# Kernel optimization log

Hardware: AMD Instinct MI355X
Metric: run time of the kernel (lower is better)

The kernel has to match this reference:

```python
import jax, jax.numpy as jnp
import numpy as np

EPS = 1e-5
INV_SQRT2 = 0.7071067811865476

def _rmsnorm(x, w):
    rms = jnp.sqrt(jnp.sum(x * x, axis=-1) / x.shape[-1] + EPS)
    return x / rms[..., None] * w

def _gelu(x):
    # exact erf-based GELU as in the torch module
    return x * (1.0 + jax.scipy.special.erf(x * INV_SQRT2)) * 0.5

def setup_inputs() -> dict:
    key = jax.random.key(0)
    ks = jax.random.split(key, 8)
    B, S, D, DFF = 4, 2048, 1024, 4096
    s = 0.02  # realistic init scale keeps softmax non-degenerate
    return {
        "x": jax.random.normal(ks[0], (B, S, D), jnp.float32),
        "ln1": jax.random.uniform(ks[1], (D,), jnp.float32),
        "ln2": jax.random.uniform(ks[2], (D,), jnp.float32),
        "ffn1": jax.random.normal(ks[3], (DFF, D), jnp.float32) * s,
        "ffn2": jax.random.normal(ks[4], (D, DFF), jnp.float32) * s,
        "k_proj": jax.random.normal(ks[5], (D, D), jnp.float32) * s,
        "q_proj": jax.random.normal(ks[6], (D, D), jnp.float32) * s,
        "v_proj": jax.random.normal(ks[7], (D, D), jnp.float32) * s,
        "out_proj": jax.random.normal(jax.random.fold_in(key, 99), (D, D), jnp.float32) * s,
    }

def reference(x, ln1, ln2, ffn1, ffn2, k_proj, q_proj, v_proj, out_proj):
    S = x.shape[1]
    d_k = x.shape[-1]
    # --- attention branch (single-head, as in source) ---
    h = _rmsnorm(x, ln1)
    Q = h @ q_proj.T  # [B,S,D]
    K = h @ k_proj.T
    V = h @ v_proj.T
    scores = jnp.einsum('bqd,bkd->bqk', Q, K) / jnp.sqrt(jnp.float32(d_k))
    attn = jax.nn.softmax(scores, axis=-1)
    # source: softmax first, then zero out strict-upper (future) entries, renormalize
    causal = jnp.tril(jnp.ones((S, S), jnp.float32))
    attn = attn * causal
    attn = attn / jnp.sum(attn, axis=-1, keepdims=True)
    mh = jnp.einsum('bqk,bkd->bqd', attn, V) @ out_proj
    y = x + mh
    # --- FFN branch: NOTE source feeds RMSNorm2(x), not y ---
    h2 = _rmsnorm(x, ln2)
    ff = _gelu(h2 @ ffn1.T) @ ffn2.T
    return y + ff
```

## Files before the change

### kernel.cpp

```cpp
#include <hip/hip_runtime.h>
#include <math.h>

typedef __bf16 bf16_t;
typedef __bf16 bf16x8 __attribute__((ext_vector_type(8)));
typedef float f32x4 __attribute__((ext_vector_type(4)));

#define LDS16(g, l) __builtin_amdgcn_global_load_lds( \
    (__attribute__((address_space(1))) void*)(g),     \
    (__attribute__((address_space(3))) void*)(l), 16, 0, 0)

__global__ __launch_bounds__(256) void prep_kernel(
    const float* __restrict__ qp, const float* __restrict__ kp,
    const float* __restrict__ vp, const float* __restrict__ f1,
    const float* __restrict__ f2, const float* __restrict__ op,
    const float* __restrict__ x, const float* __restrict__ ln1,
    bf16_t* __restrict__ qkvb, bf16_t* __restrict__ f1b,
    bf16_t* __restrict__ f2b, bf16_t* __restrict__ opT,
    bf16_t* __restrict__ h1)
{
    __shared__ float tile[32][33];
    __shared__ float red[4];
    int bid = blockIdx.x;
    int t = threadIdx.x;
    if (bid < 11264) {
        size_t i = ((size_t)bid * 256 + t) * 4;
        const float* src;
        bf16_t* dst;
        if (i < 3145728) {
            if (i < 1048576)      { src = qp + i;             dst = qkvb + i; }
            else if (i < 2097152) { src = kp + (i - 1048576); dst = qkvb + i; }
            else                  { src = vp + (i - 2097152); dst = qkvb + i; }
        } else if (i < 7340032) { src = f1 + (i - 3145728); dst = f1b + (i - 3145728); }
        else                    { src = f2 + (i - 7340032); dst = f2b + (i - 7340032); }
        float4 v = *(const float4*)src;
        dst[0] = (bf16_t)v.x; dst[1] = (bf16_t)v.y;
        dst[2] = (bf16_t)v.z; dst[3] = (bf16_t)v.w;
    } else if (bid < 12288) {
        int b2 = bid - 11264;
        int c0 = (b2 & 31) * 32, r0 = (b2 >> 5) * 32;
        int tx = t & 31, ty = t >> 5;
#pragma unroll
        for (int i = 0; i < 32; i += 8)
            tile[ty + i][tx] = op[(size_t)(r0 + ty + i) * 1024 + c0 + tx];
        __syncthreads();
#pragma unroll
        for (int i = 0; i < 32; i += 8)
            opT[(size_t)(c0 + ty + i) * 1024 + r0 + tx] = (bf16_t)tile[tx][ty + i];
    } else {
        int row = bid - 12288;
        float4 xv = ((const float4*)(x + (size_t)row * 1024))[t];
        float ss = xv.x * xv.x + xv.y * xv.y + xv.z * xv.z + xv.w * xv.w;
#pragma unroll
        for (int o = 32; o > 0; o >>= 1) ss += __shfl_xor(ss, o, 64);
        if ((t & 63) == 0) red[t >> 6] = ss;
        __syncthreads();
        ss = red[0] + red[1] + red[2] + red[3];
        float rinv = rsqrtf(ss * (1.0f / 1024.0f) + 1e-5f);
        float4 wv = ((const float4*)ln1)[t];
        bf16_t* hp = h1 + (size_t)row * 1024 + t * 4;
        hp[0] = (bf16_t)(xv.x * rinv * wv.x);
        hp[1] = (bf16_t)(xv.y * rinv * wv.y);
        hp[2] = (bf16_t)(xv.z * rinv * wv.z);
        hp[3] = (bf16_t)(xv.w * rinv * wv.w);
    }
}

__global__ __launch_bounds__(256) void rmsnorm_kernel(
    const float* __restrict__ x, const float* __restrict__ w,
    bf16_t* __restrict__ h)
{
    int row = blockIdx.x;
    int t = threadIdx.x;
    float4 xv = ((const float4*)(x + (size_t)row * 1024))[t];
    float ss = xv.x * xv.x + xv.y * xv.y + xv.z * xv.z + xv.w * xv.w;
#pragma unroll
    for (int o = 32; o > 0; o >>= 1) ss += __shfl_xor(ss, o, 64);
    __shared__ float red[4];
    if ((t & 63) == 0) red[t >> 6] = ss;
    __syncthreads();
    ss = red[0] + red[1] + red[2] + red[3];
    float rinv = rsqrtf(ss * (1.0f / 1024.0f) + 1e-5f);
    float4 wv = ((const float4*)w)[t];
    bf16_t* hp = h + (size_t)row * 1024 + t * 4;
    hp[0] = (bf16_t)(xv.x * rinv * wv.x);
    hp[1] = (bf16_t)(xv.y * rinv * wv.y);
    hp[2] = (bf16_t)(xv.z * rinv * wv.z);
    hp[3] = (bf16_t)(xv.w * rinv * wv.w);
}

__global__ __launch_bounds__(256) void transpose_bf16(
    const bf16_t* __restrict__ in, bf16_t* __restrict__ out,
    int rows, int ldin, long long sIn, long long sOut)
{
    __shared__ bf16_t tile[32][33];
    int b = blockIdx.z;
    const bf16_t* ip = in + (long long)b * sIn;
    bf16_t* op = out + (long long)b * sOut;
    int c0 = blockIdx.x * 32, r0 = blockIdx.y * 32;
    int tx = threadIdx.x & 31, ty = threadIdx.x >> 5;
#pragma unroll
    for (int i = 0; i < 32; i += 8)
        tile[ty + i][tx] = ip[(size_t)(r0 + ty + i) * ldin + c0 + tx];
    __syncthreads();
#pragma unroll
    for (int i = 0; i < 32; i += 8)
        op[(size_t)(c0 + ty + i) * rows + r0 + tx] = tile[tx][ty + i];
}

__global__ __launch_bounds__(256) void causal_softmax_kernel(bf16_t* __restrict__ SP)
{
    const int S = 2048;
    int q = blockIdx.x, b = blockIdx.y;
    bf16_t* row = SP + ((size_t)b * S + q) * S;
    int t = threadIdx.x;
    int j0 = t * 8;
    int Jstore = ((q >> 7) + 1) << 7;

    float v[8];
    if (j0 + 7 <= q) {
        bf16x8 xv = *(const bf16x8*)(row + j0);
#pragma unroll
        for (int i = 0; i < 8; i++) v[i] = (float)xv[i];
    } else if (j0 <= q) {
#pragma unroll
        for (int i = 0; i < 8; i++)
            v[i] = (j0 + i <= q) ? (float)row[j0 + i] : -1e30f;
    } else {
#pragma unroll
        for (int i = 0; i < 8; i++) v[i] = -1e30f;
    }

    float mx = v[0];
#pragma unroll
    for (int i = 1; i < 8; i++) mx = fmaxf(mx, v[i]);
#pragma unroll
    for (int o = 32; o > 0; o >>= 1) mx = fmaxf(mx, __shfl_xor(mx, o, 64));
    __shared__ float sm[4], ssum[4];
    if ((t & 63) == 0) sm[t >> 6] = mx;
    __syncthreads();
    mx = fmaxf(fmaxf(sm[0], sm[1]), fmaxf(sm[2], sm[3]));

    float e[8];
    float sum = 0.f;
#pragma unroll
    for (int i = 0; i < 8; i++) {
        e[i] = (v[i] > -1e29f) ? expf(v[i] - mx) : 0.f;
        sum += e[i];
    }
#pragma unroll
    for (int o = 32; o > 0; o >>= 1) sum += __shfl_xor(sum, o, 64);
    if ((t & 63) == 0) ssum[t >> 6] = sum;
    __syncthreads();
    sum = ssum[0] + ssum[1] + ssum[2] + ssum[3];
    float r = 1.0f / sum;

    if (j0 < Jstore) {
        bf16x8 ov;
#pragma unroll
        for (int i = 0; i < 8; i++) ov[i] = (bf16_t)(e[i] * r);
        *(bf16x8*)(row + j0) = ov;
    }
}

template <int EPI, bool CSKIP, bool CKLOOP, bool ASPLIT>
__global__ __launch_bounds__(256) void gemm_bt(
    const bf16_t* __restrict__ A, const bf16_t* __restrict__ A2, int lda,
    const bf16_t* __restrict__ B, int ldb,
    void* Cv, int ldc, const float* R,
    int K, int Ksp, int Mt, long long sA, long long sB, long long sC,
    float scale)
{
    int id = blockIdx.x, bz = blockIdx.z;
    int xcd = id & 7, p = id >> 3;
    int chunk = Mt >> 3;
    int bm = xcd * chunk + (p % chunk);
    int bn = p / chunk;
    if (CSKIP && bn > bm) return;

    __shared__ __align__(16) bf16_t At[128 * 64];
    __shared__ __align__(16) bf16_t Bt[128 * 64];
    int t = threadIdx.x;
    int w = t >> 6, l = t & 63;
    int wm = w >> 1, wn = w & 1;
    int lane_m = l & 15, quad = l >> 4;

    const bf16_t* Ag = A + (long long)bz * sA + (size_t)(bm * 128) * lda;
    const bf16_t* Bg = B + (long long)bz * sB + (size_t)(bn * 128) * ldb;

    int Keff = K;
    if (CKLOOP) {
        int kk = (bm + 1) * 128;
        if (kk < K) Keff = kk;
    }

    f32x4 acc[4][4] = {};

    int rb = w * 8 + (l >> 3);
    int g0 = ((l & 7) ^ ((l >> 3) & 7)) * 8;
    const bf16_t* a0[4];
    const bf16_t* a1[4];
    const bf16_t* b0[4];
#pragma unroll
    for (int j = 0; j < 4; j++) {
        size_t ro = (size_t)(rb + 32 * j);
        a0[j] = Ag + ro * lda + g0;
        if (ASPLIT) a1[j] = A2 + (long long)bz * sA + (size_t)(bm * 128) * lda
                           + ro * lda + g0;
        b0[j] = Bg + ro * ldb + g0;
    }

    int s0 = (quad ^ (lane_m & 7)) * 8;
    int s1 = ((4 + quad) ^ (lane_m & 7)) * 8;

    for (int kt = 0; kt < Keff; kt += 64) {
        __syncthreads();
#pragma unroll
        for (int j = 0; j < 4; j++) {
            const bf16_t* pa = a0[j] + kt;
            if (ASPLIT && kt >= Ksp) pa = a1[j] + (kt - Ksp);
            LDS16(pa, At + (size_t)w * 512 + j * 2048);
            LDS16(b0[j] + kt, Bt + (size_t)w * 512 + j * 2048);
        }
        __syncthreads();

#pragma unroll
        for (int h = 0; h < 2; h++) {
            int sh = h ? s1 : s0;
            bf16x8 af[4], bfr[4];
#pragma unroll
            for (int mi = 0; mi < 4; mi++)
                af[mi] = *(const bf16x8*)(At + (wm * 64 + mi * 16 + lane_m) * 64 + sh);
#pragma unroll
            for (int ni = 0; ni < 4; ni++)
                bfr[ni] = *(const bf16x8*)(Bt + (wn * 64 + ni * 16 + lane_m) * 64 + sh);
#pragma unroll
            for (int mi = 0; mi < 4; mi++)
#pragma unroll
                for (int ni = 0; ni < 4; ni++)
                    acc[mi][ni] = __builtin_amdgcn_mfma_f32_16x16x32_bf16(
                        af[mi], bfr[ni], acc[mi][ni], 0, 0, 0);
        }
    }

    long long cbase = (long long)bz * sC;
#pragma unroll
    for (int mi = 0; mi < 4; mi++) {
#pragma unroll
        for (int r = 0; r < 4; r++) {
            int row = bm * 128 + wm * 64 + mi * 16 + quad * 4 + r;
#pragma unroll
            for (int ni = 0; ni < 4; ni++) {
                int col = bn * 128 + wn * 64 + ni * 16 + lane_m;
                float v = acc[mi][ni][r];
                size_t idx = (size_t)(cbase + (long long)row * ldc + col);
                if (EPI == 0) {
                    ((bf16_t*)Cv)[idx] = (bf16_t)(v * scale);
                } else if (EPI == 1) {
                    float g = 0.5f * v * (1.0f + erff(v * 0.70710678118654752f));
                    ((bf16_t*)Cv)[idx] = (bf16_t)g;
                } else {
                    float rv = R[(size_t)row * ldc + col];
                    ((float*)Cv)[idx] = v + rv;
                }
            }
        }
    }
}

extern "C" void kernel_launch(void* const* d_in, const int* in_sizes, int n_in,
                              void* d_out, int out_size, void* d_ws, size_t ws_size,
                              hipStream_t stream)
{
    (void)in_sizes; (void)n_in; (void)out_size;
    const float* x    = (const float*)d_in[0];
    const float* ln1  = (const float*)d_in[1];
    const float* ln2  = (const float*)d_in[2];
    const float* ffn1 = (const float*)d_in[3];
    const float* ffn2 = (const float*)d_in[4];
    const float* kp   = (const float*)d_in[5];
    const float* qp   = (const float*)d_in[6];
    const float* vp   = (const float*)d_in[7];
    const float* op   = (const float*)d_in[8];
    float* out = (float*)d_out;

    const size_t MiB = 1048576;
    char* ws = (char*)d_ws;
    bf16_t* qkvb = (bf16_t*)(ws + 0 * MiB);
    bf16_t* opT  = (bf16_t*)(ws + 6 * MiB);
    bf16_t* f1b  = (bf16_t*)(ws + 8 * MiB);
    bf16_t* f2b  = (bf16_t*)(ws + 16 * MiB);
    bf16_t* h1   = (bf16_t*)(ws + 24 * MiB);
    bf16_t* VT   = (bf16_t*)(ws + 24 * MiB);
    bf16_t* h2   = (bf16_t*)(ws + 24 * MiB);
    bf16_t* QKVb = (bf16_t*)(ws + 40 * MiB);
    bf16_t* AV   = (bf16_t*)(ws + 40 * MiB);
    bf16_t* G0   = (bf16_t*)(ws + 40 * MiB);
    bf16_t* G1   = (bf16_t*)(ws + 72 * MiB);
    bf16_t* SP   = (bf16_t*)d_out;
    bool bigws = ws_size >= 104 * MiB;

    dim3 blk(256);
    const int HUGE_K = 1 << 30;

    prep_kernel<<<dim3(20480), blk, 0, stream>>>(
        qp, kp, vp, ffn1, ffn2, op, x, ln1, qkvb, f1b, f2b, opT, h1);

    gemm_bt<0, false, false, false><<<dim3(1536), blk, 0, stream>>>(
        h1, h1, 1024, qkvb, 1024, QKVb, 3072, nullptr,
        1024, HUGE_K, 64, 0, 0, 0, 1.0f);

    gemm_bt<0, true, false, false><<<dim3(256, 1, 4), blk, 0, stream>>>(
        QKVb, QKVb, 3072, QKVb + 1024, 3072, SP, 2048, nullptr,
        1024, HUGE_K, 16,
        (long long)2048 * 3072, (long long)2048 * 3072, (long long)2048 * 2048,
        1.0f / 32.0f);

    transpose_bf16<<<dim3(32, 64, 4), blk, 0, stream>>>(
        QKVb + 2048, VT, 2048, 3072,
        (long long)2048 * 3072, (long long)1024 * 2048);

    causal_softmax_kernel<<<dim3(2048, 4), blk, 0, stream>>>(SP);

    gemm_bt<0, false, true, false><<<dim3(128, 1, 4), blk, 0, stream>>>(
        SP, SP, 2048, VT, 2048, AV, 1024, nullptr,
        2048, HUGE_K, 16,
        (long long)2048 * 2048, (long long)1024 * 2048, (long long)2048 * 1024,
        1.0f);

    gemm_bt<2, false, false, false><<<dim3(512), blk, 0, stream>>>(
        AV, AV, 1024, opT, 1024, out, 1024, x,
        1024, HUGE_K, 64, 0, 0, 0, 1.0f);

    rmsnorm_kernel<<<dim3(8192), blk, 0, stream>>>(x, ln2, h2);

    if (bigws) {
        gemm_bt<1, false, false, false><<<dim3(1024), blk, 0, stream>>>(
            h2, h2, 1024, f1b, 1024, G0, 2048, nullptr,
            1024, HUGE_K, 64, 0, 0, 0, 1.0f);
        gemm_bt<1, false, false, false><<<dim3(1024), blk, 0, stream>>>(
            h2, h2, 1024, f1b + (size_t)2048 * 1024, 1024, G1, 2048, nullptr,
            1024, HUGE_K, 64, 0, 0, 0, 1.0f);
        gemm_bt<2, false, false, true><<<dim3(512), blk, 0, stream>>>(
            G0, G1, 2048, f2b, 4096, out, 1024, out,
            4096, 2048, 64, 0, 0, 0, 1.0f);
    } else {
        for (int half = 0; half < 2; half++) {
            gemm_bt<1, false, false, false><<<dim3(1024), blk, 0, stream>>>(
                h2, h2, 1024, f1b + (size_t)half * 2048 * 1024, 1024, G0, 2048,
                nullptr, 1024, HUGE_K, 64, 0, 0, 0, 1.0f);
            gemm_bt<2, false, false, false><<<dim3(512), blk, 0, stream>>>(
                G0, G0, 2048, f2b + half * 2048, 4096, out, 1024, out,
                2048, HUGE_K, 64, 0, 0, 0, 1.0f);
        }
    }
}
```

Baseline: 544.0 us.

## Launch only lower-triangular score tiles and remap GEMM tiles across XCDs by N

The causal QK^T GEMM now launches only the 136 lower-triangular tiles per batch, decoding (bm, bn) from a triangular index, so the grid no longer includes early-exiting upper blocks. The block-to-tile mapping for the other GEMMs changes to spread N tiles across XCDs, with M as the slow index. The FFN up-projection becomes a single GEMM writing a contiguous 4096-wide G buffer, which removes the split-A path. This trims idle block launches and tail imbalance, and the new XCD mapping changes L2 reuse patterns, which may help or hurt.

New measurement: 545.9 us. Within noise of the previous version (+0.4%).

```diff
diff --git a/kernel.cpp b/kernel.cpp
--- a/kernel.cpp
+++ b/kernel.cpp
@@ -162,20 +162,27 @@
     }
 }
 
-template <int EPI, bool CSKIP, bool CKLOOP, bool ASPLIT>
+template <int EPI, bool TRI, bool CKLOOP>
 __global__ __launch_bounds__(256) void gemm_bt(
-    const bf16_t* __restrict__ A, const bf16_t* __restrict__ A2, int lda,
-    const bf16_t* __restrict__ B, int ldb,
+    const bf16_t* __restrict__ A, int lda, const bf16_t* __restrict__ B, int ldb,
     void* Cv, int ldc, const float* R,
-    int K, int Ksp, int Mt, long long sA, long long sB, long long sC,
-    float scale)
-{
-    int id = blockIdx.x, bz = blockIdx.z;
-    int xcd = id & 7, p = id >> 3;
-    int chunk = Mt >> 3;
-    int bm = xcd * chunk + (p % chunk);
-    int bn = p / chunk;
-    if (CSKIP && bn > bm) return;
+    int K, int Nt, long long sA, long long sB, long long sC, float scale)
+{
+    int bz = blockIdx.z;
+    int bm, bn;
+    if (TRI) {
+        int i = blockIdx.x;
+        bm = (int)((sqrtf(8.0f * i + 1.0f) - 1.0f) * 0.5f);
+        while ((bm + 1) * (bm + 2) / 2 <= i) bm++;
+        while (bm * (bm + 1) / 2 > i) bm--;
+        bn = i - bm * (bm + 1) / 2;
+    } else {
+        int id = blockIdx.x;
+        int xcd = id & 7, p = id >> 3;
+        int cn = Nt >> 3;
+        bn = xcd * cn + p % cn;
+        bm = p / cn;
+    }
 
     __shared__ __align__(16) bf16_t At[128 * 64];
     __shared__ __align__(16) bf16_t Bt[128 * 64];
@@ -198,14 +205,11 @@
     int rb = w * 8 + (l >> 3);
     int g0 = ((l & 7) ^ ((l >> 3) & 7)) * 8;
     const bf16_t* a0[4];
-    const bf16_t* a1[4];
     const bf16_t* b0[4];
 #pragma unroll
     for (int j = 0; j < 4; j++) {
         size_t ro = (size_t)(rb + 32 * j);
         a0[j] = Ag + ro * lda + g0;
-        if (ASPLIT) a1[j] = A2 + (long long)bz * sA + (size_t)(bm * 128) * lda
-                           + ro * lda + g0;
         b0[j] = Bg + ro * ldb + g0;
     }
 
@@ -216,9 +220,7 @@
         __syncthreads();
 #pragma unroll
         for (int j = 0; j < 4; j++) {
-            const bf16_t* pa = a0[j] + kt;
-            if (ASPLIT && kt >= Ksp) pa = a1[j] + (kt - Ksp);
-            LDS16(pa, At + (size_t)w * 512 + j * 2048);
+            LDS16(a0[j] + kt, At + (size_t)w * 512 + j * 2048);
             LDS16(b0[j] + kt, Bt + (size_t)w * 512 + j * 2048);
         }
         __syncthreads();
@@ -294,24 +296,20 @@
     bf16_t* h2   = (bf16_t*)(ws + 24 * MiB);
     bf16_t* QKVb = (bf16_t*)(ws + 40 * MiB);
     bf16_t* AV   = (bf16_t*)(ws + 40 * MiB);
-    bf16_t* G0   = (bf16_t*)(ws + 40 * MiB);
-    bf16_t* G1   = (bf16_t*)(ws + 72 * MiB);
+    bf16_t* G    = (bf16_t*)(ws + 40 * MiB);
     bf16_t* SP   = (bf16_t*)d_out;
     bool bigws = ws_size >= 104 * MiB;
 
     dim3 blk(256);
-    const int HUGE_K = 1 << 30;
 
     prep_kernel<<<dim3(20480), blk, 0, stream>>>(
         qp, kp, vp, ffn1, ffn2, op, x, ln1, qkvb, f1b, f2b, opT, h1);
 
-    gemm_bt<0, false, false, false><<<dim3(1536), blk, 0, stream>>>(
-        h1, h1, 1024, qkvb, 1024, QKVb, 3072, nullptr,
-        1024, HUGE_K, 64, 0, 0, 0, 1.0f);
-
-    gemm_bt<0, true, false, false><<<dim3(256, 1, 4), blk, 0, stream>>>(
-        QKVb, QKVb, 3072, QKVb + 1024, 3072, SP, 2048, nullptr,
-        1024, HUGE_K, 16,
+    gemm_bt<0, false, false><<<dim3(1536), blk, 0, stream>>>(
+        h1, 1024, qkvb, 1024, QKVb, 3072, nullptr, 1024, 24, 0, 0, 0, 1.0f);
+
+    gemm_bt<0, true, false><<<dim3(136, 1, 4), blk, 0, stream>>>(
+        QKVb, 3072, QKVb + 1024, 3072, SP, 2048, nullptr, 1024, 16,
         (long long)2048 * 3072, (long long)2048 * 3072, (long long)2048 * 2048,
         1.0f / 32.0f);
 
@@ -321,36 +319,29 @@
 
     causal_softmax_kernel<<<dim3(2048, 4), blk, 0, stream>>>(SP);
 
-    gemm_bt<0, false, true, false><<<dim3(128, 1, 4), blk, 0, stream>>>(
-        SP, SP, 2048, VT, 2048, AV, 1024, nullptr,
-        2048, HUGE_K, 16,
+    gemm_bt<0, false, true><<<dim3(128, 1, 4), blk, 0, stream>>>(
+        SP, 2048, VT, 2048, AV, 1024, nullptr, 2048, 8,
         (long long)2048 * 2048, (long long)1024 * 2048, (long long)2048 * 1024,
         1.0f);
 
-    gemm_bt<2, false, false, false><<<dim3(512), blk, 0, stream>>>(
-        AV, AV, 1024, opT, 1024, out, 1024, x,
-        1024, HUGE_K, 64, 0, 0, 0, 1.0f);
+    gemm_bt<2, false, false><<<dim3(512), blk, 0, stream>>>(
+        AV, 1024, opT, 1024, out, 1024, x, 1024, 8, 0, 0, 0, 1.0f);
 
     rmsnorm_kernel<<<dim3(8192), blk, 0, stream>>>(x, ln2, h2);
 
     if (bigws) {
-        gemm_bt<1, false, false, false><<<dim3(1024), blk, 0, stream>>>(
-            h2, h2, 1024, f1b, 1024, G0, 2048, nullptr,
-            1024, HUGE_K, 64, 0, 0, 0, 1.0f);
-        gemm_bt<1, false, false, false><<<dim3(1024), blk, 0, stream>>>(
-            h2, h2, 1024, f1b + (size_t)2048 * 1024, 1024, G1, 2048, nullptr,
-            1024, HUGE_K, 64, 0, 0, 0, 1.0f);
-        gemm_bt<2, false, false, true><<<dim3(512), blk, 0, stream>>>(
-            G0, G1, 2048, f2b, 4096, out, 1024, out,
-            4096, 2048, 64, 0, 0, 0, 1.0f);
+        gemm_bt<1, false, false><<<dim3(2048), blk, 0, stream>>>(
+            h2, 1024, f1b, 1024, G, 4096, nullptr, 1024, 32, 0, 0, 0, 1.0f);
+        gemm_bt<2, false, false><<<dim3(512), blk, 0, stream>>>(
+            G, 4096, f2b, 4096, out, 1024, out, 4096, 8, 0, 0, 0, 1.0f);
     } else {
         for (int half = 0; half < 2; half++) {
-            gemm_bt<1, false, false, false><<<dim3(1024), blk, 0, stream>>>(
-                h2, h2, 1024, f1b + (size_t)half * 2048 * 1024, 1024, G0, 2048,
-                nullptr, 1024, HUGE_K, 64, 0, 0, 0, 1.0f);
-            gemm_bt<2, false, false, false><<<dim3(512), blk, 0, stream>>>(
-                G0, G0, 2048, f2b + half * 2048, 4096, out, 1024, out,
-                2048, HUGE_K, 64, 0, 0, 0, 1.0f);
+            gemm_bt<1, false, false><<<dim3(1024), blk, 0, stream>>>(
+                h2, 1024, f1b + (size_t)half * 2048 * 1024, 1024, G, 2048,
+                nullptr, 1024, 16, 0, 0, 0, 1.0f);
+            gemm_bt<2, false, false><<<dim3(512), blk, 0, stream>>>(
+                G, 2048, f2b + half * 2048, 4096, out, 1024, out,
+                2048, 8, 0, 0, 0, 1.0f);
         }
     }
 }
```
